# Kernel tuning notes

Measured on AMD Instinct MI355X. Metric: run time of the kernel, lower is better.

Reference implementation:

```python
import jax, jax.numpy as jnp
import numpy as np
from jax import lax

B, T, U, V = 4, 200, 100, 1024
D_ENC, D_DEC, J = 144, 320, 320


def setup_inputs() -> dict:
    key = jax.random.key(0)
    ks = jax.random.split(key, 8)
    s = lambda d: 1.0 / np.sqrt(d).astype(np.float32)
    return {
        "enc_out": jax.random.normal(ks[0], (B, T, D_ENC), jnp.float32),
        "dec_out": jax.random.normal(ks[1], (B, U + 1, D_DEC), jnp.float32),
        "W_enc": jax.random.normal(ks[2], (D_ENC, J), jnp.float32) * s(D_ENC),
        "b_enc": jnp.zeros((J,), jnp.float32),
        "W_dec": jax.random.normal(ks[3], (D_DEC, J), jnp.float32) * s(D_DEC),
        "b_dec": jnp.zeros((J,), jnp.float32),
        "W_out": jax.random.normal(ks[4], (J, V), jnp.float32) * s(J),
        "b_out": jnp.zeros((V,), jnp.float32),
        "targets": jax.random.randint(ks[5], (B, U), 1, V, jnp.int32),
        "enc_lengths": jax.random.randint(ks[6], (B,), T // 2, T + 1, jnp.int32),
        "target_lengths": jax.random.randint(ks[7], (B,), U // 2, U + 1, jnp.int32),
    }


def _rnnt_loss(log_probs, targets, enc_lengths, target_lengths):
    # log_probs: [B, T, U+1, V]; blank index = 0 (matches RNNTLoss(blank=0))
    blank_lp = log_probs[..., 0]  # [B, T, U+1]
    idx = jnp.broadcast_to(targets[:, None, :, None].astype(jnp.int32), (B, T, U, 1))
    emit_lp = jnp.take_along_axis(log_probs[:, :, :U, :], idx, axis=-1)[..., 0]  # [B, T, U]

    # alpha[0, u] = sum of emit log-probs along u at t=0
    alpha0 = jnp.concatenate(
        [jnp.zeros((B, 1), log_probs.dtype), jnp.cumsum(emit_lp[:, 0, :], axis=1)], axis=1
    )  # [B, U+1]

    def row(a, emit_t):
        # a: alpha_prev + blank (vertical transitions), [B, U+1]; emit_t: [B, U]
        def step(prev, xs):
            a_u, e_prev = xs
            cur = jnp.logaddexp(a_u, prev + e_prev)
            return cur, cur
        _, rest = lax.scan(step, a[:, 0], (a[:, 1:].T, emit_t.T))  # rest: [U, B]
        return jnp.concatenate([a[:, :1], rest.T], axis=1)

    def t_step(alpha_prev, xs):
        blank_prev, emit_t = xs
        alpha_t = row(alpha_prev + blank_prev, emit_t)
        return alpha_t, alpha_t

    xs = (jnp.swapaxes(blank_lp[:, :-1, :], 0, 1), jnp.swapaxes(emit_lp[:, 1:, :], 0, 1))
    _, alphas_rest = lax.scan(t_step, alpha0, xs)  # [T-1, B, U+1]
    alphas = jnp.concatenate([alpha0[None], alphas_rest], axis=0)  # [T, B, U+1]

    b_idx = jnp.arange(B)
    t_idx = enc_lengths - 1
    ll = alphas[t_idx, b_idx, target_lengths] + blank_lp[b_idx, t_idx, target_lengths]
    return jnp.mean(-ll)  # reduction='mean' over batch


def reference(enc_out, dec_out, W_enc, b_enc, W_dec, b_dec, W_out, b_out, targets, enc_lengths, target_lengths):
    enc_p = enc_out @ W_enc + b_enc  # [B, T, J]
    dec_p = dec_out @ W_dec + b_dec  # [B, U+1, J]
    joint = jnp.tanh(enc_p[:, :, None, :] + dec_p[:, None, :, :])  # [B, T, U+1, J]
    logits = joint @ W_out + b_out  # [B, T, U+1, V]
    log_probs = jax.nn.log_softmax(logits, axis=-1)
    return _rnnt_loss(log_probs, targets, enc_lengths, target_lengths)
```

## Files before the change

kernel.cpp:

```cpp
#include <hip/hip_runtime.h>
#include <hip/hip_bf16.h>
#include <math.h>

#define B_ 4
#define T_ 200
#define U_ 100
#define V_ 1024
#define DE 144
#define DD 320
#define J_ 320
#define M_TOT (B_ * T_ * (U_ + 1))
#define SSTR 328
#define DSTR 104
#define NDIAG 300
#define LOG2E 1.4426950408889634f

typedef __attribute__((ext_vector_type(8))) short bf16x8_t;
typedef __attribute__((ext_vector_type(4))) float f32x4_t;

__device__ __forceinline__ float fast_tanh(float x) {
    float e = exp2f(x * (2.0f * LOG2E));
    float r = __frcp_rn(e + 1.0f);
    return fmaf(-2.0f, r, 1.0f);
}

__device__ __forceinline__ ushort f2bf(float x) {
    uint u = __float_as_uint(x);
    uint r = (u + 0x7FFFu + ((u >> 16) & 1u)) >> 16;
    return (ushort)r;
}

__global__ __launch_bounds__(320) void prep_kernel(
    const float* __restrict__ enc_out, const float* __restrict__ dec_out,
    const float* __restrict__ W_enc, const float* __restrict__ b_enc,
    const float* __restrict__ W_dec, const float* __restrict__ b_dec,
    const float* __restrict__ W_out,
    float* __restrict__ enc_p, float* __restrict__ dec_p,
    ushort* __restrict__ Wt) {
    const int bid = blockIdx.x;
    const int tid = threadIdx.x;
    if (bid < 1204) {
        __shared__ float sx[320];
        const float* X; const float* W; const float* bias; float* Y;
        int K, r;
        if (bid < 800) { X = enc_out; W = W_enc; bias = b_enc; Y = enc_p; K = DE; r = bid; }
        else           { X = dec_out; W = W_dec; bias = b_dec; Y = dec_p; K = DD; r = bid - 800; }
        for (int k = tid; k < K; k += 320) sx[k] = X[r * K + k];
        __syncthreads();
        float acc = bias[tid];
#pragma unroll 4
        for (int k = 0; k < K; k++) acc = fmaf(sx[k], W[k * J_ + tid], acc);
        Y[r * J_ + tid] = acc;
    } else {
        int idx = (bid - 1204) * 320 + tid;
        int k = idx >> 10;
        int v = idx & 1023;
        ushort b = f2bf(W_out[idx]);
        int frag = (v >> 4) * 10 + (k >> 5);
        int lane = (v & 15) | (((k >> 3) & 3) << 4);
        int elem = k & 7;
        Wt[frag * 512 + lane * 8 + elem] = b;
    }
}

__global__ __launch_bounds__(1024, 4) void joint_mfma(
    const float* __restrict__ enc_p, const float* __restrict__ dec_p,
    const ushort* __restrict__ Wt, const float* __restrict__ b_out,
    const int* __restrict__ targets,
    float* __restrict__ bsk, float* __restrict__ esk) {
    __shared__ ushort sh[64 * SSTR];
    __shared__ float partm[16][64];
    __shared__ float parts[16][64];
    __shared__ float lse_sh[64];
    __shared__ int tgt_sh[64];

    const int tid = threadIdx.x;
    const int r0 = blockIdx.x * 64;

    {
        const int si = tid >> 4;
        const int sq = tid & 15;
        int rc = r0 + si;
        if (rc > M_TOT - 1) rc = M_TOT - 1;
        int b = rc / 20200;
        int rem = rc - b * 20200;
        int t = rem / 101;
        int u = rem - t * 101;
        const float4* ep = (const float4*)&enc_p[(b * 200 + t) * 320];
        const float4* dp = (const float4*)&dec_p[(b * 101 + u) * 320];
        ushort* shp = &sh[si * SSTR];
#pragma unroll
        for (int it = 0; it < 5; it++) {
            int kq = sq + it * 16;
            float4 e = ep[kq];
            float4 dd = dp[kq];
            float t0 = fast_tanh(e.x + dd.x);
            float t1 = fast_tanh(e.y + dd.y);
            float t2 = fast_tanh(e.z + dd.z);
            float t3 = fast_tanh(e.w + dd.w);
            __hip_bfloat162 p0 = __float22bfloat162_rn(make_float2(t0, t1));
            __hip_bfloat162 p1 = __float22bfloat162_rn(make_float2(t2, t3));
            uint2 pk;
            pk.x = *(uint*)&p0;
            pk.y = *(uint*)&p1;
            *(uint2*)&shp[kq * 4] = pk;
        }
    }
    if (tid < 64) {
        int rc = r0 + tid;
        int tg = -1;
        if (rc < M_TOT) {
            int b = rc / 20200;
            int rem = rc - b * 20200;
            int u = rem - (rem / 101) * 101;
            if (u < U_) tg = targets[b * U_ + u];
        }
        tgt_sh[tid] = tg;
    }
    __syncthreads();

    const int wave = tid >> 6;
    const int lane = tid & 63;
    const int lrow = lane & 15;
    const int lk = (lane >> 4) * 8;
    const int cb16 = wave * 4;

    f32x4_t acc[4][4];
#pragma unroll
    for (int mt = 0; mt < 4; mt++)
#pragma unroll
        for (int nt = 0; nt < 4; nt++) acc[mt][nt] = (f32x4_t)(0.0f);

    for (int ks = 0; ks < 10; ks++) {
        bf16x8_t a[4];
#pragma unroll
        for (int mt = 0; mt < 4; mt++)
            a[mt] = *(const bf16x8_t*)&sh[(mt * 16 + lrow) * SSTR + ks * 32 + lk];
#pragma unroll
        for (int nt = 0; nt < 4; nt++) {
            bf16x8_t bfr = *(const bf16x8_t*)&Wt[(((cb16 + nt) * 10 + ks) << 9) + lane * 8];
#pragma unroll
            for (int mt = 0; mt < 4; mt++)
                acc[mt][nt] = __builtin_amdgcn_mfma_f32_16x16x32_bf16(a[mt], bfr, acc[mt][nt], 0, 0, 0);
        }
    }

    float bo[4];
#pragma unroll
    for (int nt = 0; nt < 4; nt++) bo[nt] = b_out[wave * 64 + nt * 16 + lrow];
#pragma unroll
    for (int mt = 0; mt < 4; mt++)
#pragma unroll
        for (int nt = 0; nt < 4; nt++) acc[mt][nt] += bo[nt];

#pragma unroll
    for (int mt = 0; mt < 4; mt++) {
#pragma unroll
        for (int j = 0; j < 4; j++) {
            float m = fmaxf(fmaxf(acc[mt][0][j], acc[mt][1][j]),
                            fmaxf(acc[mt][2][j], acc[mt][3][j]));
#pragma unroll
            for (int off = 1; off < 16; off <<= 1)
                m = fmaxf(m, __shfl_xor(m, off, 16));
            float mm = m * LOG2E;
            float s = exp2f(fmaf(acc[mt][0][j], LOG2E, -mm));
            s += exp2f(fmaf(acc[mt][1][j], LOG2E, -mm));
            s += exp2f(fmaf(acc[mt][2][j], LOG2E, -mm));
            s += exp2f(fmaf(acc[mt][3][j], LOG2E, -mm));
#pragma unroll
            for (int off = 1; off < 16; off <<= 1)
                s += __shfl_xor(s, off, 16);
            if (lrow == 0) {
                int row = mt * 16 + (lane >> 4) * 4 + j;
                partm[wave][row] = m;
                parts[wave][row] = s;
            }
        }
    }
    __syncthreads();
    if (tid < 64) {
        float m = partm[0][tid];
        float s = parts[0][tid];
#pragma unroll
        for (int w = 1; w < 16; w++) {
            float mo = partm[w][tid], so = parts[w][tid];
            float M = fmaxf(m, mo);
            s = s * __expf(m - M) + so * __expf(mo - M);
            m = M;
        }
        lse_sh[tid] = m + __logf(s);
    }
    __syncthreads();

#pragma unroll
    for (int mt = 0; mt < 4; mt++) {
#pragma unroll
        for (int j = 0; j < 4; j++) {
            int lr = mt * 16 + (lane >> 4) * 4 + j;
            int r = r0 + lr;
            if (r >= M_TOT) continue;
            int tc = tgt_sh[lr];
            bool isblank = (wave == 0) && (lrow == 0);
            bool isemit = (tc >= 0) && ((tc >> 6) == wave) && ((tc & 15) == lrow);
            if (isblank || isemit) {
                int b = r / 20200;
                int rem = r - b * 20200;
                int t = rem / 101;
                int u = rem - t * 101;
                float lse = lse_sh[lr];
                if (isblank)
                    bsk[(b * NDIAG + t + u) * DSTR + u] = acc[mt][0][j] - lse;
                if (isemit) {
                    int ntl = (tc >> 4) & 3;
                    float v = acc[mt][0][j];
#pragma unroll
                    for (int nt = 1; nt < 4; nt++)
                        if (nt == ntl) v = acc[mt][nt][j];
                    esk[(b * NDIAG + t + u) * DSTR + u] = v - lse;
                }
            }
        }
    }
}

__global__ __launch_bounds__(256) void alpha4_kernel(
    const float* __restrict__ bsk, const float* __restrict__ esk,
    const int* __restrict__ enc_len, const int* __restrict__ tgt_len,
    float* __restrict__ out) {
    __shared__ float ll_sh[B_];
    const int tid = threadIdx.x;
    const int b = tid >> 6;
    const int l = tid & 63;
    const float* Bp = bsk + b * (NDIAG * DSTR);
    const float* Ep = esk + b * (NDIAG * DSTR);
    const int el = enc_len[b];
    const int tl = tgt_len[b];
    const int dfin = el - 1 + tl;

    float a1 = (l == 0) ? 0.0f : -INFINITY;
    float a2 = -INFINITY;

    float rb1[4], rb2[4], re1[4], re2[4];
#pragma unroll
    for (int k = 0; k < 4; k++) {
        rb1[k] = Bp[k * DSTR + l];
        rb2[k] = Bp[k * DSTR + 64 + l];
        re1[k] = Ep[k * DSTR + l];
        re2[k] = Ep[k * DSTR + 64 + l];
    }

    for (int dc = 1; dc <= 297; dc += 4) {
#pragma unroll
        for (int q = 0; q < 4; q++) {
            const int d = dc + q;
            if (d > NDIAG - 1) continue;
            const int sc = (d - 1) & 3;
            const int sm = d & 3;
            float cb1 = rb1[sc], cb2 = rb2[sc], ce1 = re1[sc], ce2 = re2[sc];
            float mb1 = rb1[sm], mb2 = rb2[sm];
            int dn = d + 3;
            if (dn > NDIAG - 1) dn = NDIAG - 1;
            rb1[sc] = Bp[dn * DSTR + l];
            rb2[sc] = Bp[dn * DSTR + 64 + l];
            re1[sc] = Ep[dn * DSTR + l];
            re2[sc] = Ep[dn * DSTR + 64 + l];

            float pe1 = __shfl_up(ce1, 1, 64);
            float e1hi = __shfl(ce1, 63, 64);
            float pe2s = __shfl_up(ce2, 1, 64);
            float pe2 = (l == 0) ? e1hi : pe2s;
            float pa1 = __shfl_up(a1, 1, 64);
            float a1hi = __shfl(a1, 63, 64);
            float pa2s = __shfl_up(a2, 1, 64);
            float pa2 = (l == 0) ? a1hi : pa2s;

            const int t1 = d - l;
            float va = a1 + cb1;
            float vb = (l >= 1) ? pa1 + pe1 : -INFINITY;
            float M = fmaxf(va, vb);
            float v1 = (M == -INFINITY)
                           ? -INFINITY
                           : M + __logf(1.0f + __expf(fminf(va, vb) - M));
            if (t1 < 0 || t1 >= T_ || l > U_) v1 = -INFINITY;

            const int t2 = d - 64 - l;
            float va2 = a2 + cb2;
            float vb2 = pa2 + pe2;
            float M2 = fmaxf(va2, vb2);
            float v2 = (M2 == -INFINITY)
                           ? -INFINITY
                           : M2 + __logf(1.0f + __expf(fminf(va2, vb2) - M2));
            if (t2 < 0 || t2 >= T_ || (64 + l) > U_) v2 = -INFINITY;

            if (d == dfin) {
                if (l == tl) ll_sh[b] = v1 + mb1;
                if (64 + l == tl) ll_sh[b] = v2 + mb2;
            }
            a1 = v1;
            a2 = v2;
        }
    }
    __syncthreads();
    if (tid == 0)
        out[0] = -0.25f * (ll_sh[0] + ll_sh[1] + ll_sh[2] + ll_sh[3]);
}

extern "C" void kernel_launch(void* const* d_in, const int* in_sizes, int n_in,
                              void* d_out, int out_size, void* d_ws, size_t ws_size,
                              hipStream_t stream) {
    const float* enc_out = (const float*)d_in[0];
    const float* dec_out = (const float*)d_in[1];
    const float* W_enc = (const float*)d_in[2];
    const float* b_enc = (const float*)d_in[3];
    const float* W_dec = (const float*)d_in[4];
    const float* b_dec = (const float*)d_in[5];
    const float* W_out = (const float*)d_in[6];
    const float* b_out = (const float*)d_in[7];
    const int* targets = (const int*)d_in[8];
    const int* enc_len = (const int*)d_in[9];
    const int* tgt_len = (const int*)d_in[10];

    float* ws = (float*)d_ws;
    float* enc_p = ws;
    float* dec_p = enc_p + B_ * T_ * J_;
    float* bsk = dec_p + B_ * (U_ + 1) * J_;
    float* esk = bsk + B_ * NDIAG * DSTR;
    ushort* Wt = (ushort*)(esk + B_ * NDIAG * DSTR);

    prep_kernel<<<2228, 320, 0, stream>>>(enc_out, dec_out, W_enc, b_enc,
                                          W_dec, b_dec, W_out, enc_p, dec_p, Wt);

    joint_mfma<<<(M_TOT + 63) / 64, 1024, 0, stream>>>(
        enc_p, dec_p, Wt, b_out, targets, bsk, esk);

    alpha4_kernel<<<1, 256, 0, stream>>>(bsk, esk, enc_len, tgt_len, (float*)d_out);
}
```

Before: 218.0 us.

## Register-block projection GEMV, deepen alpha prefetch, prioritize MFMA issue

The encoder/decoder projections now process 16 rows per 640-thread block, so each weight load is reused across 8 rows in registers instead of one row per block. The alpha recurrence kernel prefetches 8 diagonals ahead instead of 4 to hide global-load latency in the serial chain. The joint kernel raises wave priority around MFMA bursts and issues the target loads before the tanh staging. The changes trade more registers and fewer, larger prep blocks for fewer redundant weight reads and less latency exposure.

```diff
diff --git a/kernel.cpp b/kernel.cpp
--- a/kernel.cpp
+++ b/kernel.cpp
@@ -30,29 +30,65 @@
     return (ushort)r;
 }
 
-__global__ __launch_bounds__(320) void prep_kernel(
+template <int K>
+__device__ __forceinline__ void proj_body(const float* __restrict__ X,
+                                          const float* __restrict__ W,
+                                          const float* __restrict__ bias,
+                                          float* __restrict__ Y,
+                                          int r0, int R, float* sx, int tid) {
+    constexpr int QK = K / 4;
+    for (int q = tid; q < 16 * QK; q += 640) {
+        int row = q / QK;
+        int kq = q - row * QK;
+        int r = r0 + row;
+        if (r >= R) r = R - 1;
+        *(float4*)&sx[row * K + kq * 4] = *(const float4*)&X[r * K + kq * 4];
+    }
+    __syncthreads();
+    const int half = (tid >= 320) ? 1 : 0;
+    const int c = tid - half * 320;
+    float acc[8];
+#pragma unroll
+    for (int i = 0; i < 8; i++) acc[i] = 0.0f;
+    for (int k = 0; k < K; k += 4) {
+        float w0 = W[(k + 0) * 320 + c];
+        float w1 = W[(k + 1) * 320 + c];
+        float w2 = W[(k + 2) * 320 + c];
+        float w3 = W[(k + 3) * 320 + c];
+#pragma unroll
+        for (int i = 0; i < 8; i++) {
+            const float4 x4 = *(const float4*)&sx[(half * 8 + i) * K + k];
+            acc[i] = fmaf(x4.x, w0, acc[i]);
+            acc[i] = fmaf(x4.y, w1, acc[i]);
+            acc[i] = fmaf(x4.z, w2, acc[i]);
+            acc[i] = fmaf(x4.w, w3, acc[i]);
+        }
+    }
+    const float bb = bias[c];
+#pragma unroll
+    for (int i = 0; i < 8; i++) {
+        int r = r0 + half * 8 + i;
+        if (r < R) Y[r * 320 + c] = acc[i] + bb;
+    }
+}
+
+__global__ __launch_bounds__(640) void prep_kernel(
     const float* __restrict__ enc_out, const float* __restrict__ dec_out,
     const float* __restrict__ W_enc, const float* __restrict__ b_enc,
     const float* __restrict__ W_dec, const float* __restrict__ b_dec,
     const float* __restrict__ W_out,
     float* __restrict__ enc_p, float* __restrict__ dec_p,
     ushort* __restrict__ Wt) {
+    __shared__ float sx[16 * 320];
     const int bid = blockIdx.x;
     const int tid = threadIdx.x;
-    if (bid < 1204) {
-        __shared__ float sx[320];
-        const float* X; const float* W; const float* bias; float* Y;
-        int K, r;
-        if (bid < 800) { X = enc_out; W = W_enc; bias = b_enc; Y = enc_p; K = DE; r = bid; }
-        else           { X = dec_out; W = W_dec; bias = b_dec; Y = dec_p; K = DD; r = bid - 800; }
-        for (int k = tid; k < K; k += 320) sx[k] = X[r * K + k];
-        __syncthreads();
-        float acc = bias[tid];
-#pragma unroll 4
-        for (int k = 0; k < K; k++) acc = fmaf(sx[k], W[k * J_ + tid], acc);
-        Y[r * J_ + tid] = acc;
+    if (bid < 50) {
+        proj_body<DE>(enc_out, W_enc, b_enc, enc_p, bid * 16, B_ * T_, sx, tid);
+    } else if (bid < 76) {
+        proj_body<DD>(dec_out, W_dec, b_dec, dec_p, (bid - 50) * 16,
+                      B_ * (U_ + 1), sx, tid);
     } else {
-        int idx = (bid - 1204) * 320 + tid;
+        int idx = (bid - 76) * 640 + tid;
         int k = idx >> 10;
         int v = idx & 1023;
         ushort b = f2bf(W_out[idx]);
@@ -76,6 +112,18 @@
 
     const int tid = threadIdx.x;
     const int r0 = blockIdx.x * 64;
+
+    if (tid < 64) {
+        int rc = r0 + tid;
+        int tg = -1;
+        if (rc < M_TOT) {
+            int b = rc / 20200;
+            int rem = rc - b * 20200;
+            int u = rem - (rem / 101) * 101;
+            if (u < U_) tg = targets[b * U_ + u];
+        }
+        tgt_sh[tid] = tg;
+    }
 
     {
         const int si = tid >> 4;
@@ -106,17 +154,6 @@
             *(uint2*)&shp[kq * 4] = pk;
         }
     }
-    if (tid < 64) {
-        int rc = r0 + tid;
-        int tg = -1;
-        if (rc < M_TOT) {
-            int b = rc / 20200;
-            int rem = rc - b * 20200;
-            int u = rem - (rem / 101) * 101;
-            if (u < U_) tg = targets[b * U_ + u];
-        }
-        tgt_sh[tid] = tg;
-    }
     __syncthreads();
 
     const int wave = tid >> 6;
@@ -139,9 +176,11 @@
 #pragma unroll
         for (int nt = 0; nt < 4; nt++) {
             bf16x8_t bfr = *(const bf16x8_t*)&Wt[(((cb16 + nt) * 10 + ks) << 9) + lane * 8];
+            __builtin_amdgcn_s_setprio(1);
 #pragma unroll
             for (int mt = 0; mt < 4; mt++)
                 acc[mt][nt] = __builtin_amdgcn_mfma_f32_16x16x32_bf16(a[mt], bfr, acc[mt][nt], 0, 0, 0);
+            __builtin_amdgcn_s_setprio(0);
         }
     }
 
@@ -223,7 +262,7 @@
     }
 }
 
-__global__ __launch_bounds__(256) void alpha4_kernel(
+__global__ __launch_bounds__(256) void alpha8_kernel(
     const float* __restrict__ bsk, const float* __restrict__ esk,
     const int* __restrict__ enc_len, const int* __restrict__ tgt_len,
     float* __restrict__ out) {
@@ -240,25 +279,25 @@
     float a1 = (l == 0) ? 0.0f : -INFINITY;
     float a2 = -INFINITY;
 
-    float rb1[4], rb2[4], re1[4], re2[4];
-#pragma unroll
-    for (int k = 0; k < 4; k++) {
+    float rb1[8], rb2[8], re1[8], re2[8];
+#pragma unroll
+    for (int k = 0; k < 8; k++) {
         rb1[k] = Bp[k * DSTR + l];
         rb2[k] = Bp[k * DSTR + 64 + l];
         re1[k] = Ep[k * DSTR + l];
         re2[k] = Ep[k * DSTR + 64 + l];
     }
 
-    for (int dc = 1; dc <= 297; dc += 4) {
-#pragma unroll
-        for (int q = 0; q < 4; q++) {
+    for (int dc = 1; dc <= 297; dc += 8) {
+#pragma unroll
+        for (int q = 0; q < 8; q++) {
             const int d = dc + q;
             if (d > NDIAG - 1) continue;
-            const int sc = (d - 1) & 3;
-            const int sm = d & 3;
+            const int sc = q;
+            const int sm = (q + 1) & 7;
             float cb1 = rb1[sc], cb2 = rb2[sc], ce1 = re1[sc], ce2 = re2[sc];
             float mb1 = rb1[sm], mb2 = rb2[sm];
-            int dn = d + 3;
+            int dn = d + 7;
             if (dn > NDIAG - 1) dn = NDIAG - 1;
             rb1[sc] = Bp[dn * DSTR + l];
             rb2[sc] = Bp[dn * DSTR + 64 + l];
@@ -327,11 +366,11 @@
     float* esk = bsk + B_ * NDIAG * DSTR;
     ushort* Wt = (ushort*)(esk + B_ * NDIAG * DSTR);
 
-    prep_kernel<<<2228, 320, 0, stream>>>(enc_out, dec_out, W_enc, b_enc,
-                                          W_dec, b_dec, W_out, enc_p, dec_p, Wt);
+    prep_kernel<<<588, 640, 0, stream>>>(enc_out, dec_out, W_enc, b_enc,
+                                         W_dec, b_dec, W_out, enc_p, dec_p, Wt);
 
     joint_mfma<<<(M_TOT + 63) / 64, 1024, 0, stream>>>(
         enc_p, dec_p, Wt, b_out, targets, bsk, esk);
 
-    alpha4_kernel<<<1, 256, 0, stream>>>(bsk, esk, enc_len, tgt_len, (float*)d_out);
-}
+    alpha8_kernel<<<1, 256, 0, stream>>>(bsk, esk, enc_len, tgt_len, (float*)d_out);
+}
```

Measured after the change: 228.6 us. 4.9% more time.
